# Performance work log

Measured on AMD Instinct MI355X. Metric: run time of the kernel, lower is better.

The kernel has to match this reference:

```python
import jax, jax.numpy as jnp
import numpy as np

HEADS = 8


def pe_table(length, d):
    # standard sinusoidal positional encoding [length, d]
    pos = jnp.arange(length, dtype=jnp.float32)[:, None]
    div = jnp.exp(jnp.arange(0, d, 2, dtype=jnp.float32) * (-np.log(10000.0) / d))
    ang = pos * div
    pe = jnp.zeros((length, d), jnp.float32)
    pe = pe.at[:, 0::2].set(jnp.sin(ang)).at[:, 1::2].set(jnp.cos(ang))
    return pe


def layernorm(x, a, b, eps=1e-6):
    mu = x.mean(-1, keepdims=True)
    sd = jnp.std(x, axis=-1, ddof=1, keepdims=True)  # torch .std() is unbiased
    return a * (x - mu) / (sd + eps) + b


def setup_inputs() -> dict:
    key = jax.random.key(0)
    ks = jax.random.split(key, 16)
    B, N, T, L = 8, 8, 512, 512
    ts_c, ts_e = 64, 192
    aux_c, aux_e = 16, 64
    edge_c = 8
    d = 256
    s = 0.02
    w = lambda k, shape: jax.random.normal(k, shape, jnp.float32) * s
    return {
        'x': jax.random.normal(ks[0], (B, T, d), jnp.float32),
        'nbr_ts': jax.random.normal(ks[1], (B, N, ts_c, L), jnp.float32),
        'nbr_aux': jax.random.normal(ks[2], (B, N, aux_c, L), jnp.float32),
        'nbr_edge': jax.random.normal(ks[3], (B, N, edge_c, T), jnp.float32),
        'attn_mask': jax.random.randint(ks[4], (B, N, 1, L), 0, 2).astype(jnp.int32),
        'Wts': w(ks[5], (ts_e, ts_c)), 'bts': jnp.zeros((ts_e,), jnp.float32),
        'Waux': w(ks[6], (aux_e, aux_c)), 'baux': jnp.zeros((aux_e,), jnp.float32),
        'Wedge': w(ks[7], (d, edge_c)), 'bedge': jnp.zeros((d,), jnp.float32),
        'ln_a': jnp.ones((d,), jnp.float32), 'ln_b': jnp.zeros((d,), jnp.float32),
        'Wq': w(ks[8], (d, d)), 'bq': jnp.zeros((d,), jnp.float32),
        'Wk': w(ks[9], (d, d)), 'bk': jnp.zeros((d,), jnp.float32),
        'Wv': w(ks[10], (d, d)), 'bv': jnp.zeros((d,), jnp.float32),
        'Wo': w(ks[11], (d, d)), 'bo': jnp.zeros((d,), jnp.float32),
    }


def reference(x, nbr_ts, nbr_aux, nbr_edge, attn_mask,
              Wts, bts, Waux, baux, Wedge, bedge, ln_a, ln_b,
              Wq, bq, Wk, bk, Wv, bv, Wo, bo):
    B, T, d = x.shape
    N, L = nbr_ts.shape[1], nbr_ts.shape[-1]
    h = HEADS
    dk = d // h

    x_pe = x + pe_table(T, d)                                   # [B,T,d]

    # per-neighbor projections (transpose channel-first inputs, then Linear)
    ts_emb = jnp.einsum('bncl,ec->bnle', nbr_ts, Wts) + bts     # [B,N,L,ts_e]
    aux_emb = jnp.einsum('bncl,ec->bnle', nbr_aux, Waux) + baux # [B,N,L,aux_e]
    kv = jnp.concatenate([ts_emb, aux_emb], axis=-1)            # [B,N,L,d]
    kv = kv + pe_table(L, d)

    # SublayerConnection: x + cross_attn(norm(x), kv, kv, mask)
    q_in = layernorm(x_pe, ln_a, ln_b)
    q = (q_in @ Wq.T + bq).reshape(B, T, h, dk).transpose(0, 2, 1, 3)  # [B,h,T,dk]
    k = (kv @ Wk.T + bk).reshape(B, N, L, h, dk)
    v = (kv @ Wv.T + bv).reshape(B, N, L, h, dk)

    scores = jnp.einsum('bhtd,bnlhd->bnhtl', q, k) / jnp.sqrt(jnp.float32(dk))
    mask = attn_mask[:, :, None, :, :]                          # [B,N,1,1,L]
    scores = jnp.where(mask == 0, jnp.float32(-1e9), scores)
    p = jax.nn.softmax(scores, axis=-1)
    ctx = jnp.einsum('bnhtl,bnlhd->bnthd', p, v).reshape(B, N, T, d)
    attn = ctx @ Wo.T + bo                                      # [B,N,T,d]

    sub_out = x_pe[:, None, :, :] + attn                        # residual, [B,N,T,d]

    edge = jnp.einsum('bnct,dc->bntd', nbr_edge, Wedge) + bedge # [B,N,T,d]
    return (sub_out * edge).mean(axis=1)                        # mean over neighbors
```

## Files before the change

kernel.cpp:

```cpp
#include <hip/hip_runtime.h>
#include <hip/hip_bf16.h>
#include <math.h>

typedef __attribute__((ext_vector_type(8))) short bf16x8;
typedef __attribute__((ext_vector_type(4))) short bf16x4;
typedef __attribute__((ext_vector_type(4))) float f32x4;

__device__ __forceinline__ short f2bf(float f) {
    return (short)__builtin_bit_cast(unsigned short, __float2bfloat16(f));
}
__device__ __forceinline__ float bf2f(short s) {
    return __builtin_bit_cast(float, ((unsigned)(unsigned short)s) << 16);
}
__device__ __forceinline__ unsigned pk2bf(float a, float b) {
    return ((unsigned)(unsigned short)f2bf(b) << 16) |
           (unsigned)(unsigned short)f2bf(a);
}

#if defined(__has_builtin)
#if __has_builtin(__builtin_amdgcn_mfma_f32_16x16x16bf16_1k)
#define HAVE_MFMA16 1
#endif
#endif

__device__ __forceinline__ f32x4 mfma16(bf16x4 a, bf16x4 b, f32x4 c) {
#ifdef HAVE_MFMA16
    return __builtin_amdgcn_mfma_f32_16x16x16bf16_1k(a, b, c, 0, 0, 0);
#else
    f32x4 d;
    asm volatile("v_mfma_f32_16x16x16_bf16 %0, %1, %2, %3"
                 : "=v"(d) : "v"(a), "v"(b), "v"(c));
    return d;
#endif
}

#define SCALE2 0.25503482403f

__global__ __launch_bounds__(512) void setup_kernel(
    const float* __restrict__ Wq, const float* __restrict__ Wk,
    const float* __restrict__ Wv, const float* __restrict__ Wo,
    const float* __restrict__ Wts, const float* __restrict__ Waux,
    const float* __restrict__ bts, const float* __restrict__ baux,
    const float* __restrict__ bk, const float* __restrict__ bv,
    const float* __restrict__ x, const float* __restrict__ ln_a,
    const float* __restrict__ ln_b, const int* __restrict__ mask,
    short* __restrict__ wout, short* __restrict__ W2,
    float* __restrict__ bias2, float* __restrict__ bkv,
    float* __restrict__ pe, int* __restrict__ pos, int* __restrict__ cnt,
    short* __restrict__ xpe_bf, short* __restrict__ qin) {
    __shared__ float redA[8];
    __shared__ float redB[8];
    __shared__ int wsum[8];
    int bid = blockIdx.x, tid = threadIdx.x;
    if (bid < 128) {
        int i = bid * 512 + tid;
        wout[i]          = f2bf(Wq[i]);
        wout[65536 + i]  = f2bf(Wk[i]);
        wout[131072 + i] = f2bf(Wv[i]);
        wout[196608 + i] = f2bf(Wo[i]);
    } else if (bid < 176) {
        int idx = (bid - 128) * 512 + tid;
        int e = idx / 96, ch = idx - e * 96;
        float v = 0.f;
        if (ch < 64) { if (e < 192) v = Wts[e * 64 + ch]; }
        else if (ch < 80) { if (e >= 192) v = Waux[(e - 192) * 16 + (ch - 64)]; }
        W2[idx] = f2bf(v);
        if (idx < 256) bias2[idx] = idx < 192 ? bts[idx] : baux[idx - 192];
        if (idx < 512) bkv[idx] = idx < 256 ? bk[idx] : bv[idx - 256];
    } else if (bid < 432) {
        int t = (bid - 176) * 2 + (tid >> 8);
        int dd = tid & 255;
        int i = dd >> 1;
        float div = expf((float)(2 * i) * (-9.210340371976184f / 256.0f));
        float ang = (float)t * div;
        pe[t * 256 + dd] = (dd & 1) ? cosf(ang) : sinf(ang);
    } else if (bid < 496) {
        int bn = bid - 432;
        int lane = tid & 63, wid = tid >> 6;
        int m = mask[bn * 512 + tid] != 0;
        int v = m;
#pragma unroll
        for (int off = 1; off < 64; off <<= 1) {
            int t = __shfl_up(v, off);
            if (lane >= off) v += t;
        }
        if (lane == 63) wsum[wid] = v;
        __syncthreads();
        int base = 0;
#pragma unroll
        for (int w = 0; w < 8; ++w) base += (w < wid) ? wsum[w] : 0;
        pos[bn * 512 + tid] = m ? (base + v - 1) : -1;
        if (tid == 511) cnt[bn] = base + v;
    } else {
        int half = tid >> 8;
        int d = tid & 255;
        int row = (bid - 496) * 2 + half;
        int t = row & 511;
        int i = d >> 1;
        float div = expf((float)(2 * i) * (-9.210340371976184f / 256.0f));
        float ang = (float)t * div;
        float pev = (d & 1) ? cosf(ang) : sinf(ang);
        float v = x[(size_t)row * 256 + d] + pev;
        xpe_bf[(size_t)row * 256 + d] = f2bf(v);
        float s = v;
#pragma unroll
        for (int off = 32; off > 0; off >>= 1) s += __shfl_xor(s, off);
        if ((tid & 63) == 0) redA[tid >> 6] = s;
        __syncthreads();
        int rb = half * 4;
        float mu = (redA[rb] + redA[rb + 1] + redA[rb + 2] + redA[rb + 3]) *
                   (1.0f / 256.0f);
        float dv = v - mu;
        float s2 = dv * dv;
#pragma unroll
        for (int off = 32; off > 0; off >>= 1) s2 += __shfl_xor(s2, off);
        if ((tid & 63) == 0) redB[tid >> 6] = s2;
        __syncthreads();
        float var = (redB[rb] + redB[rb + 1] + redB[rb + 2] + redB[rb + 3]) *
                    (1.0f / 255.0f);
        float sd = sqrtf(var);
        qin[(size_t)row * 256 + d] = f2bf(ln_a[d] * dv / (sd + 1e-6f) + ln_b[d]);
    }
}

__global__ __launch_bounds__(512, 2) void kv_gemm(
    const float* __restrict__ nbr_ts, const float* __restrict__ nbr_aux,
    const short* __restrict__ W2, const float* __restrict__ bias2,
    const float* __restrict__ pe, const int* __restrict__ pos,
    short* __restrict__ kvc) {
    __shared__ __align__(16) float S1[64 * 132];
    __shared__ __align__(16) float S2[16 * 132];
    __shared__ __align__(16) short A_lds[128 * 104];
    int tid = threadIdx.x;
    int bn = blockIdx.x, l0 = blockIdx.y * 128;
    const float* tsb = nbr_ts + (size_t)bn * 64 * 512;
    const float* axb = nbr_aux + (size_t)bn * 16 * 512;
#pragma unroll
    for (int it = 0; it < 4; ++it) {
        int idx = tid + it * 512;
        int cc = idx >> 5, lq = idx & 31;
        *(float4*)&S1[cc * 132 + lq * 4] =
            *(const float4*)&tsb[(size_t)cc * 512 + l0 + lq * 4];
    }
    {
        int cc = tid >> 5, lq = tid & 31;
        *(float4*)&S2[cc * 132 + lq * 4] =
            *(const float4*)&axb[(size_t)cc * 512 + l0 + lq * 4];
    }
    __syncthreads();
#pragma unroll
    for (int p = 0; p < 3; ++p) {
        int tk = tid + p * 512;
        int l = tk & 127, chunk = tk >> 7;
        union { bf16x8 v; unsigned u[4]; } v8;
        if (chunk < 8) {
#pragma unroll
            for (int i = 0; i < 4; ++i)
                v8.u[i] = pk2bf(S1[(chunk * 8 + 2 * i) * 132 + l],
                                S1[(chunk * 8 + 2 * i + 1) * 132 + l]);
        } else if (chunk < 10) {
#pragma unroll
            for (int i = 0; i < 4; ++i)
                v8.u[i] = pk2bf(S2[((chunk - 8) * 8 + 2 * i) * 132 + l],
                                S2[((chunk - 8) * 8 + 2 * i + 1) * 132 + l]);
        } else {
#pragma unroll
            for (int i = 0; i < 4; ++i) v8.u[i] = 0;
        }
        *(bf16x8*)&A_lds[l * 104 + chunk * 8] = v8.v;
    }
    __syncthreads();
    int wid = tid >> 6, lane = tid & 63;
    int g = lane >> 4, c = lane & 15;
    int lm = wid >> 2, le = wid & 3;
    bf16x8 wf[4][3];
#pragma unroll
    for (int nf = 0; nf < 4; ++nf)
#pragma unroll
        for (int ks = 0; ks < 3; ++ks)
            wf[nf][ks] = *(const bf16x8*)&W2[(size_t)(le * 64 + nf * 16 + c) * 96 +
                                             ks * 32 + g * 8];
    f32x4 acc[4][4];
#pragma unroll
    for (int i = 0; i < 4; ++i)
#pragma unroll
        for (int j = 0; j < 4; ++j) acc[i][j] = (f32x4){0.f, 0.f, 0.f, 0.f};
#pragma unroll
    for (int ks = 0; ks < 3; ++ks) {
#pragma unroll
        for (int mf = 0; mf < 4; ++mf) {
            bf16x8 af = *(const bf16x8*)&A_lds[(lm * 64 + mf * 16 + c) * 104 +
                                               ks * 32 + g * 8];
#pragma unroll
            for (int nf = 0; nf < 4; ++nf)
                acc[mf][nf] = __builtin_amdgcn_mfma_f32_16x16x32_bf16(
                    af, wf[nf][ks], acc[mf][nf], 0, 0, 0);
        }
    }
    float b2c[4];
#pragma unroll
    for (int nf = 0; nf < 4; ++nf) b2c[nf] = bias2[le * 64 + nf * 16 + c];
    short* kvb = kvc + (size_t)bn * 512 * 256;
    const int* posb = pos + bn * 512 + l0;
#pragma unroll
    for (int mf = 0; mf < 4; ++mf) {
#pragma unroll
        for (int r = 0; r < 4; ++r) {
            int lr = lm * 64 + mf * 16 + g * 4 + r;
            int p = posb[lr];
            if (p >= 0) {
#pragma unroll
                for (int nf = 0; nf < 4; ++nf) {
                    int e = le * 64 + nf * 16 + c;
                    kvb[(size_t)p * 256 + e] =
                        f2bf(acc[mf][nf][r] + b2c[nf] +
                             pe[(size_t)(l0 + lr) * 256 + e]);
                }
            }
        }
    }
}

__global__ __launch_bounds__(256) void proj_gemm(
    const short* __restrict__ qin, const short* __restrict__ kvc,
    const short* __restrict__ wq, const short* __restrict__ wkv,
    const float* __restrict__ bq, const float* __restrict__ bkv,
    const int* __restrict__ cnt, short* __restrict__ qout,
    short* __restrict__ kv2) {
    int bx = blockIdx.x;
    const short* A; const short* Wm; const float* bias; short* C;
    int row0, col0, LDC; float esc;
    if (bx < 64) {
        row0 = (bx >> 1) * 128; col0 = (bx & 1) * 128;
        A = qin; Wm = wq; bias = bq; C = qout; LDC = 256; esc = SCALE2;
    } else {
        int idx = bx - 64;
        int bn = idx >> 4, mt = (idx >> 2) & 3, ct = idx & 3;
        int nvp = (cnt[bn] + 15) & ~15;
        row0 = mt * 128;
        if (row0 >= nvp) return;
        col0 = ct * 128;
        A = kvc + (size_t)bn * 512 * 256; Wm = wkv; bias = bkv;
        C = kv2 + (size_t)bn * 512 * 512; LDC = 512; esc = 1.0f;
    }
    __shared__ __align__(16) short As[128 * 40];
    __shared__ __align__(16) short Bs[128 * 40];
    int tid = threadIdx.x;
    int wid = tid >> 6, lane = tid & 63;
    int wm = wid >> 1, wn = wid & 1;
    int g = lane >> 4, c = lane & 15;
    f32x4 acc[4][4];
#pragma unroll
    for (int i = 0; i < 4; ++i)
#pragma unroll
        for (int j = 0; j < 4; ++j) acc[i][j] = (f32x4){0.f, 0.f, 0.f, 0.f};

    for (int k0 = 0; k0 < 256; k0 += 32) {
#pragma unroll
        for (int it = 0; it < 2; ++it) {
            int idx = tid + it * 256;
            int r = idx >> 2, ch = idx & 3;
            *(bf16x8*)&As[r * 40 + ch * 8] =
                *(const bf16x8*)&A[(size_t)(row0 + r) * 256 + k0 + ch * 8];
            *(bf16x8*)&Bs[r * 40 + ch * 8] =
                *(const bf16x8*)&Wm[(size_t)(col0 + r) * 256 + k0 + ch * 8];
        }
        __syncthreads();
        bf16x8 af[4], bfr[4];
#pragma unroll
        for (int mf = 0; mf < 4; ++mf)
            af[mf] = *(const bf16x8*)&As[(wm * 64 + mf * 16 + c) * 40 + g * 8];
#pragma unroll
        for (int nf = 0; nf < 4; ++nf)
            bfr[nf] = *(const bf16x8*)&Bs[(wn * 64 + nf * 16 + c) * 40 + g * 8];
#pragma unroll
        for (int mf = 0; mf < 4; ++mf)
#pragma unroll
            for (int nf = 0; nf < 4; ++nf)
                acc[mf][nf] = __builtin_amdgcn_mfma_f32_16x16x32_bf16(
                    af[mf], bfr[nf], acc[mf][nf], 0, 0, 0);
        __syncthreads();
    }
#pragma unroll
    for (int nf = 0; nf < 4; ++nf) {
        int col = col0 + wn * 64 + nf * 16 + c;
        float bz = bias[col];
#pragma unroll
        for (int mf = 0; mf < 4; ++mf)
#pragma unroll
            for (int r = 0; r < 4; ++r) {
                int row = row0 + wm * 64 + mf * 16 + g * 4 + r;
                C[(size_t)row * LDC + col] = f2bf((acc[mf][nf][r] + bz) * esc);
            }
    }
}

__global__ __launch_bounds__(256) void gemm_wo(
    const short* __restrict__ A, const short* __restrict__ W,
    const float* __restrict__ bias, short* __restrict__ Cout) {
    __shared__ __align__(16) short As[128 * 40];
    __shared__ __align__(16) short Bs[128 * 40];
    int tid = threadIdx.x;
    int row0 = blockIdx.x * 128, col0 = blockIdx.y * 128;
    int wid = tid >> 6, lane = tid & 63;
    int wm = wid >> 1, wn = wid & 1;
    int g = lane >> 4, c = lane & 15;
    f32x4 acc[4][4];
#pragma unroll
    for (int i = 0; i < 4; ++i)
#pragma unroll
        for (int j = 0; j < 4; ++j) acc[i][j] = (f32x4){0.f, 0.f, 0.f, 0.f};

    for (int k0 = 0; k0 < 256; k0 += 32) {
#pragma unroll
        for (int it = 0; it < 2; ++it) {
            int idx = tid + it * 256;
            int r = idx >> 2, ch = idx & 3;
            *(bf16x8*)&As[r * 40 + ch * 8] =
                *(const bf16x8*)&A[(size_t)(row0 + r) * 256 + k0 + ch * 8];
            *(bf16x8*)&Bs[r * 40 + ch * 8] =
                *(const bf16x8*)&W[(size_t)(col0 + r) * 256 + k0 + ch * 8];
        }
        __syncthreads();
        bf16x8 af[4], bfr[4];
#pragma unroll
        for (int mf = 0; mf < 4; ++mf)
            af[mf] = *(const bf16x8*)&As[(wm * 64 + mf * 16 + c) * 40 + g * 8];
#pragma unroll
        for (int nf = 0; nf < 4; ++nf)
            bfr[nf] = *(const bf16x8*)&Bs[(wn * 64 + nf * 16 + c) * 40 + g * 8];
#pragma unroll
        for (int mf = 0; mf < 4; ++mf)
#pragma unroll
            for (int nf = 0; nf < 4; ++nf)
                acc[mf][nf] = __builtin_amdgcn_mfma_f32_16x16x32_bf16(
                    af[mf], bfr[nf], acc[mf][nf], 0, 0, 0);
        __syncthreads();
    }
#pragma unroll
    for (int nf = 0; nf < 4; ++nf) {
        int col = col0 + wn * 64 + nf * 16 + c;
        float bz = bias[col];
#pragma unroll
        for (int mf = 0; mf < 4; ++mf)
#pragma unroll
            for (int r = 0; r < 4; ++r) {
                int row = row0 + wm * 64 + mf * 16 + g * 4 + r;
                Cout[(size_t)row * 256 + col] = f2bf(acc[mf][nf][r] + bz);
            }
    }
}

template <bool MASKED>
__device__ __forceinline__ void attn_step(
    const short* K_lds, const short* Vt_lds, const bf16x8* qf,
    f32x4 (*ctxa)[2], f32x4* rsv, int l0, int nv, int g, int c) {
    bf16x8 ak = *(const bf16x8*)&K_lds[(l0 + c) * 40 + g * 8];
    bf16x4 vb0 = *(const bf16x4*)&Vt_lds[c * 524 + l0 + g * 4];
    bf16x4 vb1 = *(const bf16x4*)&Vt_lds[(16 + c) * 524 + l0 + g * 4];
    int lb = l0 + g * 4;
#pragma unroll
    for (int tf = 0; tf < 4; ++tf) {
        f32x4 s = __builtin_amdgcn_mfma_f32_16x16x32_bf16(
            ak, qf[tf], (f32x4){0.f, 0.f, 0.f, 0.f}, 0, 0, 0);
        float p0 = exp2f(s[0]);
        float p1 = exp2f(s[1]);
        float p2 = exp2f(s[2]);
        float p3 = exp2f(s[3]);
        if (MASKED) {
            p0 = (lb + 0 < nv) ? p0 : 0.f;
            p1 = (lb + 1 < nv) ? p1 : 0.f;
            p2 = (lb + 2 < nv) ? p2 : 0.f;
            p3 = (lb + 3 < nv) ? p3 : 0.f;
        }
        rsv[tf] += (f32x4){p0, p1, p2, p3};
        union { bf16x4 v; unsigned u[2]; } pu;
        pu.u[0] = pk2bf(p0, p1);
        pu.u[1] = pk2bf(p2, p3);
        __builtin_amdgcn_s_setprio(1);
        ctxa[tf][0] = mfma16(pu.v, vb0, ctxa[tf][0]);
        ctxa[tf][1] = mfma16(pu.v, vb1, ctxa[tf][1]);
        __builtin_amdgcn_s_setprio(0);
    }
}

__global__ __launch_bounds__(512, 2) void attn_kernel(
    const short* __restrict__ Q, const short* __restrict__ KV2,
    const int* __restrict__ cnt, short* __restrict__ ctx) {
    __shared__ __align__(16) short K_lds[512 * 40];
    __shared__ __align__(16) short Vt_lds[32 * 524];
    int tid = threadIdx.x;
    int bx = blockIdx.x;
    int h = bx & 7, bn = bx >> 3, b = bn >> 3;
    int nv = cnt[bn];
    int nvp = (nv + 15) & ~15;
    const short* kvr = KV2 + (size_t)bn * 512 * 512 + h * 32;
#pragma unroll
    for (int it = 0; it < 4; ++it) {
        int idx = tid + it * 512;
        int i = idx >> 2, ch = idx & 3;
        if (i < nvp) {
            bf16x8 kval = (bf16x8){0, 0, 0, 0, 0, 0, 0, 0};
            bf16x8 vval = (bf16x8){0, 0, 0, 0, 0, 0, 0, 0};
            if (i < nv) {
                kval = *(const bf16x8*)&kvr[(size_t)i * 512 + ch * 8];
                vval = *(const bf16x8*)&kvr[(size_t)i * 512 + 256 + ch * 8];
            }
            *(bf16x8*)&K_lds[i * 40 + ch * 8] = kval;
#pragma unroll
            for (int k = 0; k < 8; ++k)
                Vt_lds[(ch * 8 + k) * 524 + i] = vval[k];
        }
    }
    __syncthreads();

    int wid = tid >> 6, lane = tid & 63;
    int g = lane >> 4, c = lane & 15;
    int t0 = wid * 64;
    const short* qg = Q + ((size_t)b * 512 + t0 + c) * 256 + h * 32 + g * 8;
    bf16x8 qf[4];
#pragma unroll
    for (int tf = 0; tf < 4; ++tf)
        qf[tf] = *(const bf16x8*)&qg[(size_t)tf * 16 * 256];

    f32x4 ctxa[4][2];
    f32x4 rsv[4];
#pragma unroll
    for (int tf = 0; tf < 4; ++tf) {
        ctxa[tf][0] = (f32x4){0.f, 0.f, 0.f, 0.f};
        ctxa[tf][1] = (f32x4){0.f, 0.f, 0.f, 0.f};
        rsv[tf] = (f32x4){0.f, 0.f, 0.f, 0.f};
    }
    int nfull = nv & ~15;
    for (int l0 = 0; l0 < nfull; l0 += 16)
        attn_step<false>(K_lds, Vt_lds, qf, ctxa, rsv, l0, nv, g, c);
    if (nfull < nvp)
        attn_step<true>(K_lds, Vt_lds, qf, ctxa, rsv, nfull, nv, g, c);
#ifndef HAVE_MFMA16
    asm volatile("s_nop 7\ns_nop 7");
#endif
#pragma unroll
    for (int tf = 0; tf < 4; ++tf) {
        float r = (rsv[tf][0] + rsv[tf][1]) + (rsv[tf][2] + rsv[tf][3]);
        r += __shfl_xor(r, 16);
        r += __shfl_xor(r, 32);
        float inv = 1.f / r;
#pragma unroll
        for (int rr = 0; rr < 4; ++rr) {
            float invr = __shfl(inv, (lane & 48) | (g * 4 + rr));
            ctxa[tf][0][rr] *= invr;
            ctxa[tf][1][rr] *= invr;
        }
    }
    __syncthreads();
#pragma unroll
    for (int tf = 0; tf < 4; ++tf)
#pragma unroll
        for (int df = 0; df < 2; ++df)
#pragma unroll
            for (int rr = 0; rr < 4; ++rr)
                K_lds[(t0 + tf * 16 + g * 4 + rr) * 40 + df * 16 + c] =
                    f2bf(ctxa[tf][df][rr]);
    __syncthreads();
    short* cg = ctx + (size_t)bn * 512 * 256 + h * 32;
#pragma unroll
    for (int it = 0; it < 4; ++it) {
        int idx = tid + it * 512;
        int l = idx >> 2, ch = idx & 3;
        *(bf16x8*)&cg[(size_t)l * 256 + ch * 8] =
            *(const bf16x8*)&K_lds[l * 40 + ch * 8];
    }
}

__global__ __launch_bounds__(256) void final_kernel(
    const short* __restrict__ xpe, const short* __restrict__ attn,
    const float* __restrict__ nbr_edge, const float* __restrict__ Wedge,
    const float* __restrict__ bedge, float* __restrict__ out) {
    int row = blockIdx.x;
    int tid = threadIdx.x;
    int b = row >> 9, t = row & 511;
    float xp = bf2f(xpe[(size_t)row * 256 + tid]);
    float we[8];
#pragma unroll
    for (int cc = 0; cc < 8; ++cc) we[cc] = Wedge[tid * 8 + cc];
    float be = bedge[tid];
    float acc = 0.f;
#pragma unroll
    for (int n = 0; n < 8; ++n) {
        size_t bn = (size_t)(b * 8 + n);
        float av = bf2f(attn[(bn * 512 + t) * 256 + tid]);
        float eg = be;
#pragma unroll
        for (int cc = 0; cc < 8; ++cc)
            eg = fmaf(nbr_edge[(bn * 8 + cc) * 512 + t], we[cc], eg);
        acc = fmaf(xp + av, eg, acc);
    }
    out[(size_t)row * 256 + tid] = acc * 0.125f;
}

extern "C" void kernel_launch(void* const* d_in, const int* in_sizes, int n_in,
                              void* d_out, int out_size, void* d_ws, size_t ws_size,
                              hipStream_t stream) {
    const float* x        = (const float*)d_in[0];
    const float* nbr_ts   = (const float*)d_in[1];
    const float* nbr_aux  = (const float*)d_in[2];
    const float* nbr_edge = (const float*)d_in[3];
    const int*   mask     = (const int*)d_in[4];
    const float* Wts  = (const float*)d_in[5];
    const float* bts  = (const float*)d_in[6];
    const float* Waux = (const float*)d_in[7];
    const float* baux = (const float*)d_in[8];
    const float* Wedge= (const float*)d_in[9];
    const float* bedge= (const float*)d_in[10];
    const float* ln_a = (const float*)d_in[11];
    const float* ln_b = (const float*)d_in[12];
    const float* Wq = (const float*)d_in[13];
    const float* bq = (const float*)d_in[14];
    const float* Wk = (const float*)d_in[15];
    const float* bk = (const float*)d_in[16];
    const float* Wv = (const float*)d_in[17];
    const float* bv = (const float*)d_in[18];
    const float* Wo = (const float*)d_in[19];
    const float* bo = (const float*)d_in[20];
    float* out = (float*)d_out;

    char* W = (char*)d_ws;
    float* pe_f    = (float*)(W);
    short* xpe_bf  = (short*)(W + 524288);
    short* qin_bf  = (short*)(W + 4718592);
    short* q_bf    = (short*)(W + 6815744);
    short* kvc_bf  = (short*)(W + 8912896);
    short* kv2c_bf = (short*)(W + 25690112);
    short* ctx_bf  = (short*)(W + 59244544);
    short* attn_bf = (short*)(W + 76021760);
    short* w_bf    = (short*)(W + 92798976);
    short* W2_bf   = (short*)(W + 93323264);
    float* bias2_f = (float*)(W + 93372416);
    float* bkv_f   = (float*)(W + 93373440);
    int*   pos     = (int*)  (W + 93375488);
    int*   cnt     = (int*)  (W + 93506560);
    short* wq_bf = w_bf;
    short* wkv_bf = w_bf + 65536;
    short* wo_bf = w_bf + 196608;

    setup_kernel<<<2544, 512, 0, stream>>>(
        Wq, Wk, Wv, Wo, Wts, Waux, bts, baux, bk, bv, x, ln_a, ln_b, mask,
        w_bf, W2_bf, bias2_f, bkv_f, pe_f, pos, cnt, xpe_bf, qin_bf);
    kv_gemm<<<dim3(64, 4), 512, 0, stream>>>(nbr_ts, nbr_aux, W2_bf, bias2_f,
                                             pe_f, pos, kvc_bf);
    proj_gemm<<<1088, 256, 0, stream>>>(qin_bf, kvc_bf, wq_bf, wkv_bf, bq,
                                        bkv_f, cnt, q_bf, kv2c_bf);
    attn_kernel<<<512, 512, 0, stream>>>(q_bf, kv2c_bf, cnt, ctx_bf);
    gemm_wo<<<dim3(256, 2), 256, 0, stream>>>(ctx_bf, wo_bf, bo, attn_bf);
    final_kernel<<<4096, 256, 0, stream>>>(xpe_bf, attn_bf, nbr_edge, Wedge,
                                           bedge, out);
}
```

Baseline: 114.6 us.

## Fuse Wo projection GEMM with residual, edge gating and neighbor mean

Replaces the separate Wo GEMM and final elementwise kernel with one kernel. Each block keeps a 64-column slice of Wo in LDS, loops over the 8 neighbors, computes the 32x64 attention-output tile with MFMA and immediately applies the residual, edge projection and neighbor mean in registers. This removes the bf16 attn intermediate round trip through HBM (about 16MB written and read) and one launch. The cost is smaller per-block GEMM tiles with a sync per neighbor, and Wo is re-read once per block.

```diff
diff --git a/kernel.cpp b/kernel.cpp
--- a/kernel.cpp
+++ b/kernel.cpp
@@ -295,62 +295,6 @@
     }
 }
 
-__global__ __launch_bounds__(256) void gemm_wo(
-    const short* __restrict__ A, const short* __restrict__ W,
-    const float* __restrict__ bias, short* __restrict__ Cout) {
-    __shared__ __align__(16) short As[128 * 40];
-    __shared__ __align__(16) short Bs[128 * 40];
-    int tid = threadIdx.x;
-    int row0 = blockIdx.x * 128, col0 = blockIdx.y * 128;
-    int wid = tid >> 6, lane = tid & 63;
-    int wm = wid >> 1, wn = wid & 1;
-    int g = lane >> 4, c = lane & 15;
-    f32x4 acc[4][4];
-#pragma unroll
-    for (int i = 0; i < 4; ++i)
-#pragma unroll
-        for (int j = 0; j < 4; ++j) acc[i][j] = (f32x4){0.f, 0.f, 0.f, 0.f};
-
-    for (int k0 = 0; k0 < 256; k0 += 32) {
-#pragma unroll
-        for (int it = 0; it < 2; ++it) {
-            int idx = tid + it * 256;
-            int r = idx >> 2, ch = idx & 3;
-            *(bf16x8*)&As[r * 40 + ch * 8] =
-                *(const bf16x8*)&A[(size_t)(row0 + r) * 256 + k0 + ch * 8];
-            *(bf16x8*)&Bs[r * 40 + ch * 8] =
-                *(const bf16x8*)&W[(size_t)(col0 + r) * 256 + k0 + ch * 8];
-        }
-        __syncthreads();
-        bf16x8 af[4], bfr[4];
-#pragma unroll
-        for (int mf = 0; mf < 4; ++mf)
-            af[mf] = *(const bf16x8*)&As[(wm * 64 + mf * 16 + c) * 40 + g * 8];
-#pragma unroll
-        for (int nf = 0; nf < 4; ++nf)
-            bfr[nf] = *(const bf16x8*)&Bs[(wn * 64 + nf * 16 + c) * 40 + g * 8];
-#pragma unroll
-        for (int mf = 0; mf < 4; ++mf)
-#pragma unroll
-            for (int nf = 0; nf < 4; ++nf)
-                acc[mf][nf] = __builtin_amdgcn_mfma_f32_16x16x32_bf16(
-                    af[mf], bfr[nf], acc[mf][nf], 0, 0, 0);
-        __syncthreads();
-    }
-#pragma unroll
-    for (int nf = 0; nf < 4; ++nf) {
-        int col = col0 + wn * 64 + nf * 16 + c;
-        float bz = bias[col];
-#pragma unroll
-        for (int mf = 0; mf < 4; ++mf)
-#pragma unroll
-            for (int r = 0; r < 4; ++r) {
-                int row = row0 + wm * 64 + mf * 16 + g * 4 + r;
-                Cout[(size_t)row * 256 + col] = f2bf(acc[mf][nf][r] + bz);
-            }
-    }
-}
-
 template <bool MASKED>
 __device__ __forceinline__ void attn_step(
     const short* K_lds, const short* Vt_lds, const bf16x8* qf,
@@ -472,30 +416,91 @@
     }
 }
 
-__global__ __launch_bounds__(256) void final_kernel(
-    const short* __restrict__ xpe, const short* __restrict__ attn,
+__global__ __launch_bounds__(256, 3) void wo_final(
+    const short* __restrict__ ctx, const short* __restrict__ wo,
+    const float* __restrict__ bo, const short* __restrict__ xpe,
     const float* __restrict__ nbr_edge, const float* __restrict__ Wedge,
     const float* __restrict__ bedge, float* __restrict__ out) {
-    int row = blockIdx.x;
+    __shared__ __align__(16) short Ws[64 * 264];
+    __shared__ __align__(16) short As[32 * 264];
+    __shared__ __align__(16) float edge_s[8][36];
+    int bx = blockIdx.x;
+    int b = bx >> 6, tt = (bx >> 2) & 15, dt = bx & 3;
+    int t0 = tt * 32, d0 = dt * 64;
     int tid = threadIdx.x;
-    int b = row >> 9, t = row & 511;
-    float xp = bf2f(xpe[(size_t)row * 256 + tid]);
-    float we[8];
-#pragma unroll
-    for (int cc = 0; cc < 8; ++cc) we[cc] = Wedge[tid * 8 + cc];
-    float be = bedge[tid];
-    float acc = 0.f;
-#pragma unroll
+    int wid = tid >> 6, lane = tid & 63;
+    int th = wid & 1, dh = wid >> 1;
+    int g = lane >> 4, c = lane & 15;
+
+#pragma unroll
+    for (int it = 0; it < 8; ++it) {
+        int idx = tid + it * 256;
+        int r = idx >> 5, kk = (idx & 31) * 8;
+        *(bf16x8*)&Ws[r * 264 + kk] =
+            *(const bf16x8*)&wo[(size_t)(d0 + r) * 256 + kk];
+    }
+    int trloc = th * 16 + g * 4;
+    int dcol[2];
+    float we[2][8], be[2], xb[2][4];
+#pragma unroll
+    for (int j = 0; j < 2; ++j) {
+        dcol[j] = d0 + dh * 32 + j * 16 + c;
+#pragma unroll
+        for (int cc = 0; cc < 8; ++cc) we[j][cc] = Wedge[dcol[j] * 8 + cc];
+        be[j] = bedge[dcol[j]];
+        float boj = bo[dcol[j]];
+#pragma unroll
+        for (int r = 0; r < 4; ++r)
+            xb[j][r] = bf2f(xpe[((size_t)b * 512 + t0 + trloc + r) * 256 +
+                                dcol[j]]) + boj;
+    }
+    f32x4 oacc[2] = {(f32x4){0.f, 0.f, 0.f, 0.f}, (f32x4){0.f, 0.f, 0.f, 0.f}};
+
     for (int n = 0; n < 8; ++n) {
-        size_t bn = (size_t)(b * 8 + n);
-        float av = bf2f(attn[(bn * 512 + t) * 256 + tid]);
-        float eg = be;
-#pragma unroll
-        for (int cc = 0; cc < 8; ++cc)
-            eg = fmaf(nbr_edge[(bn * 8 + cc) * 512 + t], we[cc], eg);
-        acc = fmaf(xp + av, eg, acc);
-    }
-    out[(size_t)row * 256 + tid] = acc * 0.125f;
+        int bn = b * 8 + n;
+#pragma unroll
+        for (int it = 0; it < 4; ++it) {
+            int idx = tid + it * 256;
+            int r = idx >> 5, kk = (idx & 31) * 8;
+            *(bf16x8*)&As[r * 264 + kk] =
+                *(const bf16x8*)&ctx[((size_t)bn * 512 + t0 + r) * 256 + kk];
+        }
+        {
+            int cc = tid >> 5, tl = tid & 31;
+            edge_s[cc][tl] = nbr_edge[((size_t)bn * 8 + cc) * 512 + t0 + tl];
+        }
+        __syncthreads();
+        f32x4 acc[2] = {(f32x4){0.f, 0.f, 0.f, 0.f},
+                        (f32x4){0.f, 0.f, 0.f, 0.f}};
+#pragma unroll
+        for (int k0 = 0; k0 < 8; ++k0) {
+            bf16x8 af = *(const bf16x8*)&As[(th * 16 + c) * 264 + k0 * 32 + g * 8];
+#pragma unroll
+            for (int j = 0; j < 2; ++j) {
+                bf16x8 bf = *(const bf16x8*)&Ws[(dh * 32 + j * 16 + c) * 264 +
+                                                k0 * 32 + g * 8];
+                acc[j] = __builtin_amdgcn_mfma_f32_16x16x32_bf16(af, bf, acc[j],
+                                                                 0, 0, 0);
+            }
+        }
+#pragma unroll
+        for (int j = 0; j < 2; ++j)
+#pragma unroll
+            for (int r = 0; r < 4; ++r) {
+                float e = be[j];
+#pragma unroll
+                for (int cc = 0; cc < 8; ++cc)
+                    e = fmaf(edge_s[cc][trloc + r], we[j][cc], e);
+                oacc[j][r] = fmaf(acc[j][r] + xb[j][r], e, oacc[j][r]);
+            }
+        __syncthreads();
+    }
+#pragma unroll
+    for (int j = 0; j < 2; ++j)
+#pragma unroll
+        for (int r = 0; r < 4; ++r)
+            out[((size_t)b * 512 + t0 + trloc + r) * 256 + dcol[j]] =
+                oacc[j][r] * 0.125f;
 }
 
 extern "C" void kernel_launch(void* const* d_in, const int* in_sizes, int n_in,
@@ -532,7 +537,6 @@
     short* kvc_bf  = (short*)(W + 8912896);
     short* kv2c_bf = (short*)(W + 25690112);
     short* ctx_bf  = (short*)(W + 59244544);
-    short* attn_bf = (short*)(W + 76021760);
     short* w_bf    = (short*)(W + 92798976);
     short* W2_bf   = (short*)(W + 93323264);
     float* bias2_f = (float*)(W + 93372416);
@@ -551,7 +555,6 @@
     proj_gemm<<<1088, 256, 0, stream>>>(qin_bf, kvc_bf, wq_bf, wkv_bf, bq,
                                         bkv_f, cnt, q_bf, kv2c_bf);
     attn_kernel<<<512, 512, 0, stream>>>(q_bf, kv2c_bf, cnt, ctx_bf);
-    gemm_wo<<<dim3(256, 2), 256, 0, stream>>>(ctx_bf, wo_bf, bo, attn_bf);
-    final_kernel<<<4096, 256, 0, stream>>>(xpe_bf, attn_bf, nbr_edge, Wedge,
-                                           bedge, out);
-}
+    wo_final<<<512, 256, 0, stream>>>(ctx_bf, wo_bf, bo, xpe_bf, nbr_edge,
+                                      Wedge, bedge, out);
+}
```

New measurement: 104.7 us. 8.6% less time.
